# Optimization experiments

Hardware: AMD Instinct MI355X
Metric: run time of the kernel (lower is better)

## Reference

```python
import jax, jax.numpy as jnp
import numpy as np

P_FACTOR = 3.0
EPS = 1e-12  # torch F.normalize eps


def _l2_normalize(x):
    # matches torch.nn.functional.normalize(x, dim=-1): x / max(||x||, eps)
    n = jnp.linalg.norm(x, axis=-1, keepdims=True)
    return x / jnp.maximum(n, EPS)


def setup_inputs() -> dict:
    key = jax.random.key(0)
    k1, k2, k3 = jax.random.split(key, 3)
    N, D, H, C = 8192, 16384, 256, 28
    return {
        "features": jax.random.normal(k1, (N, H), dtype=jnp.float32),
        "ex_features": jax.random.normal(k2, (D, H), dtype=jnp.float32),
        "ex_class_reps": jax.random.normal(k3, (D, C), dtype=jnp.float32),
    }


def reference(features, ex_features, ex_class_reps):
    # cosine similarity: [N, D]
    s = _l2_normalize(features) @ _l2_normalize(ex_features).T
    # power-law activation: |s|^p * sign(s)
    a = jnp.power(jnp.abs(s), P_FACTOR) * jnp.sign(s)
    intensity = a.sum(axis=1)               # [N]
    echo = a @ ex_class_reps                # [N, C]
    return (echo, intensity)
```

## Files before the change

### kernel.cpp

```cpp
#include <hip/hip_runtime.h>
#include <stdint.h>


typedef unsigned short u16;
typedef __bf16 bf16x8 __attribute__((ext_vector_type(8)));
typedef float f32x4 __attribute__((ext_vector_type(4)));
typedef unsigned short u16x4 __attribute__((ext_vector_type(4)));

#define NQ 8192
#define ND 16384
#define NH 256
#define NC 28
#define DCHUNK 1024
#define NDT 8
#define NSLOT 16

__device__ __forceinline__ u16 f2bf(float f) {
  unsigned u = __builtin_bit_cast(unsigned, f);
  u += 0x7fffu + ((u >> 16) & 1u);
  return (u16)(u >> 16);
}

__device__ __forceinline__ unsigned cvtpk(float lo, float hi) {
  unsigned r;
  asm("v_cvt_pk_bf16_f32 %0, %1, %2" : "=v"(r) : "v"(lo), "v"(hi));
  return r;
}

__device__ __forceinline__ void swap2(unsigned& x, unsigned& y) {
  asm("v_permlane32_swap_b32 %0, %1" : "+v"(x), "+v"(y));
  asm("v_permlane16_swap_b32 %0, %1" : "+v"(x), "+v"(y));
}

__device__ __forceinline__ void gload16(const void* g, void* l) {
  __builtin_amdgcn_global_load_lds(
      (__attribute__((address_space(1))) void*)g,
      (__attribute__((address_space(3))) void*)l, 16, 0, 0);
}

__global__ __launch_bounds__(256) void norm_kernel(const float* __restrict__ in,
                                                   u16* __restrict__ out, int rows) {
  const int wid = threadIdx.x >> 6, lane = threadIdx.x & 63;
  const int row = blockIdx.x * 4 + wid;
  if (row >= rows) return;
  const float4* p = (const float4*)(in + (size_t)row * NH);
  float4 v = p[lane];
  float ss = v.x * v.x + v.y * v.y + v.z * v.z + v.w * v.w;
#pragma unroll
  for (int m = 1; m <= 32; m <<= 1) ss += __shfl_xor(ss, m, 64);
  const float sc = 1.0f / fmaxf(sqrtf(ss), 1e-12f);
  u16x4 o;
  o.x = f2bf(v.x * sc); o.y = f2bf(v.y * sc);
  o.z = f2bf(v.z * sc); o.w = f2bf(v.w * sc);
  *(u16x4*)(out + (size_t)row * NH + lane * 4) = o;
}

__global__ __launch_bounds__(256) void vt_kernel(const float* __restrict__ V,
                                                 u16* __restrict__ Vt) {
  const int d = blockIdx.x * 256 + threadIdx.x;
#pragma unroll
  for (int c = 0; c < NC; ++c) Vt[(size_t)c * ND + d] = f2bf(V[(size_t)d * NC + c]);
  Vt[(size_t)28 * ND + d] = 0x3F80;
  Vt[(size_t)29 * ND + d] = 0;
  Vt[(size_t)30 * ND + d] = 0;
  Vt[(size_t)31 * ND + d] = 0;
}

__global__ __launch_bounds__(256, 2) void fused_kernel(
    const u16* __restrict__ Qn, const u16* __restrict__ Kn,
    const u16* __restrict__ Vt, float* __restrict__ ep) {
  __shared__ alignas(16) char smem[32768];
  const int tid = threadIdx.x;
  const int wid = tid >> 6;
  const int lane = tid & 63;
  const int l16 = lane & 15;
  const int lg = lane >> 4;
  const int dch = blockIdx.x & 15;
  const int ntile = blockIdx.x >> 4;
  const int qbase = ntile * 128;
  const int rowbase = qbase + wid * 32;

  bf16x8 qA[2][8];
#pragma unroll
  for (int mb = 0; mb < 2; ++mb)
#pragma unroll
    for (int ks = 0; ks < 8; ++ks)
      qA[mb][ks] = *(const bf16x8*)(Qn + (size_t)(rowbase + mb * 16 + l16) * NH +
                                    ks * 32 + lg * 8);

  f32x4 eacc[2][2];
#pragma unroll
  for (int mb = 0; mb < 2; ++mb) {
    eacc[mb][0] = f32x4{0.f, 0.f, 0.f, 0.f};
    eacc[mb][1] = f32x4{0.f, 0.f, 0.f, 0.f};
  }
  f32x4 sacc[2][8];

  auto stageK = [&](int buf, int h0, const u16* kt) {
#pragma unroll
    for (int r = 0; r < 4; ++r) {
      const int row = r * 32 + (tid >> 3);
      const int c8 = (tid & 7) ^ (row & 7);
      gload16(kt + (size_t)row * NH + h0 + c8 * 8,
              smem + buf * 16384 + r * 4096 + wid * 1024);
    }
  };

  const u16* kc = Kn + (size_t)dch * DCHUNK * NH;
  stageK(0, 0, kc);
  __syncthreads();

  for (int t = 0; t < NDT; ++t) {
    const u16* kt = kc + (size_t)t * 128 * NH;
#pragma unroll
    for (int mb = 0; mb < 2; ++mb)
#pragma unroll
      for (int nb = 0; nb < 8; ++nb) sacc[mb][nb] = f32x4{0.f, 0.f, 0.f, 0.f};

#pragma unroll
    for (int ks = 0; ks < 4; ++ks) {
      if (ks < 3) stageK((ks + 1) & 1, (ks + 1) * 64, kt);
      else if (t < NDT - 1) stageK(0, 0, kt + 128 * NH);
      const char* kbuf = smem + (ks & 1) * 16384;
#pragma unroll
      for (int k2 = 0; k2 < 2; ++k2) {
        bf16x8 B[8];
#pragma unroll
        for (int nb = 0; nb < 8; ++nb)
          B[nb] = *(const bf16x8*)(kbuf + (nb * 16 + l16) * 128 +
                                   (((k2 * 4 + lg) ^ (l16 & 7)) << 4));
#pragma unroll
        for (int mb = 0; mb < 2; ++mb)
#pragma unroll
          for (int nb = 0; nb < 8; ++nb)
            sacc[mb][nb] = __builtin_amdgcn_mfma_f32_16x16x32_bf16(
                B[nb], qA[mb][ks * 2 + k2], sacc[mb][nb], 0, 0, 0);
      }
      __syncthreads();
    }

    const int dbase = dch * DCHUNK + t * 128;
#pragma unroll
    for (int mb = 0; mb < 2; ++mb) {
#pragma unroll
      for (int tg = 0; tg < 4; ++tg) {
        f32x4 sx = sacc[mb][2 * tg];
        f32x4 sy = sacc[mb][2 * tg + 1];
        f32x4 cx = sx * sx * sx;
        f32x4 cy = sy * sy * sy;
        unsigned x0 = cvtpk(cx[0], cx[1]);
        unsigned x1 = cvtpk(cx[2], cx[3]);
        unsigned y0 = cvtpk(cy[0], cy[1]);
        unsigned y1 = cvtpk(cy[2], cy[3]);
        swap2(x0, y0);
        swap2(x1, y1);
        const int4 ai = {(int)x0, (int)x1, (int)y0, (int)y1};
        const bf16x8 aA = __builtin_bit_cast(bf16x8, ai);
#pragma unroll
        for (int cn = 0; cn < 2; ++cn) {
          const bf16x8 vBf = *(const bf16x8*)(Vt + (size_t)(cn * 16 + l16) * ND +
                                              dbase + tg * 32 + lg * 8);
          eacc[mb][cn] = __builtin_amdgcn_mfma_f32_16x16x32_bf16(
              aA, vBf, eacc[mb][cn], 0, 0, 0);
        }
      }
    }
  }

#pragma unroll
  for (int mb = 0; mb < 2; ++mb)
#pragma unroll
    for (int cn = 0; cn < 2; ++cn)
#pragma unroll
      for (int r = 0; r < 4; ++r) {
        const int row = rowbase + mb * 16 + lg * 4 + r;
        ep[((size_t)dch * NQ + row) * 32 + cn * 16 + l16] = eacc[mb][cn][r];
      }
}

__global__ __launch_bounds__(256) void reduce_kernel(const float* __restrict__ ep,
                                                     float* __restrict__ out) {
  const int g = blockIdx.x * 256 + threadIdx.x;
  const int q = g >> 5, c = g & 31;
  if (c < NC) {
    float s = 0.f;
#pragma unroll
    for (int k = 0; k < NSLOT; ++k) s += ep[((size_t)k * NQ + q) * 32 + c];
    out[(size_t)q * NC + c] = s;
  } else if (c == NC) {
    float s = 0.f;
#pragma unroll
    for (int k = 0; k < NSLOT; ++k) s += ep[((size_t)k * NQ + q) * 32 + NC];
    out[(size_t)NQ * NC + q] = s;
  }
}

extern "C" void kernel_launch(void* const* d_in, const int* in_sizes, int n_in,
                              void* d_out, int out_size, void* d_ws, size_t ws_size,
                              hipStream_t stream) {
  const float* feat = (const float*)d_in[0];
  const float* exf  = (const float*)d_in[1];
  const float* exc  = (const float*)d_in[2];
  float* out = (float*)d_out;
  char* ws = (char*)d_ws;
  u16* qn = (u16*)ws;
  u16* kn = (u16*)(ws + 4194304);
  u16* vt = (u16*)(ws + 12582912);
  float* ep = (float*)(ws + 13631488);

  norm_kernel<<<dim3(NQ / 4), dim3(256), 0, stream>>>(feat, qn, NQ);
  norm_kernel<<<dim3(ND / 4), dim3(256), 0, stream>>>(exf, kn, ND);
  vt_kernel<<<dim3(ND / 256), dim3(256), 0, stream>>>(exc, vt);
  fused_kernel<<<dim3(1024), dim3(256), 0, stream>>>(qn, kn, vt, ep);
  reduce_kernel<<<dim3(NQ * 32 / 256), dim3(256), 0, stream>>>(ep, out);
}
```

Before: 98.21 us.

## Load K operands directly from global memory instead of staging through LDS

Removes the double-buffered global_load_lds staging of K tiles into shared memory and the per-step block barriers. Each wave now reads its B fragments for the MFMA directly from global memory (relying on L1/L2 for reuse across the four waves). This drops LDS usage and synchronization, but each wave issues redundant global loads for the same K tile and loses explicit prefetch overlap, so the loop may become latency-bound.

Result: slower. 289.6 us (+194.9%).

```diff
diff --git a/kernel.cpp b/kernel.cpp
--- a/kernel.cpp
+++ b/kernel.cpp
@@ -32,12 +32,6 @@
   asm("v_permlane16_swap_b32 %0, %1" : "+v"(x), "+v"(y));
 }
 
-__device__ __forceinline__ void gload16(const void* g, void* l) {
-  __builtin_amdgcn_global_load_lds(
-      (__attribute__((address_space(1))) void*)g,
-      (__attribute__((address_space(3))) void*)l, 16, 0, 0);
-}
-
 __global__ __launch_bounds__(256) void norm_kernel(const float* __restrict__ in,
                                                    u16* __restrict__ out, int rows) {
   const int wid = threadIdx.x >> 6, lane = threadIdx.x & 63;
@@ -69,7 +63,6 @@
 __global__ __launch_bounds__(256, 2) void fused_kernel(
     const u16* __restrict__ Qn, const u16* __restrict__ Kn,
     const u16* __restrict__ Vt, float* __restrict__ ep) {
-  __shared__ alignas(16) char smem[32768];
   const int tid = threadIdx.x;
   const int wid = tid >> 6;
   const int lane = tid & 63;
@@ -77,8 +70,7 @@
   const int lg = lane >> 4;
   const int dch = blockIdx.x & 15;
   const int ntile = blockIdx.x >> 4;
-  const int qbase = ntile * 128;
-  const int rowbase = qbase + wid * 32;
+  const int rowbase = ntile * 128 + wid * 32;
 
   bf16x8 qA[2][8];
 #pragma unroll
@@ -96,19 +88,7 @@
   }
   f32x4 sacc[2][8];
 
-  auto stageK = [&](int buf, int h0, const u16* kt) {
-#pragma unroll
-    for (int r = 0; r < 4; ++r) {
-      const int row = r * 32 + (tid >> 3);
-      const int c8 = (tid & 7) ^ (row & 7);
-      gload16(kt + (size_t)row * NH + h0 + c8 * 8,
-              smem + buf * 16384 + r * 4096 + wid * 1024);
-    }
-  };
-
   const u16* kc = Kn + (size_t)dch * DCHUNK * NH;
-  stageK(0, 0, kc);
-  __syncthreads();
 
   for (int t = 0; t < NDT; ++t) {
     const u16* kt = kc + (size_t)t * 128 * NH;
@@ -118,25 +98,21 @@
       for (int nb = 0; nb < 8; ++nb) sacc[mb][nb] = f32x4{0.f, 0.f, 0.f, 0.f};
 
 #pragma unroll
-    for (int ks = 0; ks < 4; ++ks) {
-      if (ks < 3) stageK((ks + 1) & 1, (ks + 1) * 64, kt);
-      else if (t < NDT - 1) stageK(0, 0, kt + 128 * NH);
-      const char* kbuf = smem + (ks & 1) * 16384;
+    for (int ks = 0; ks < 8; ++ks) {
 #pragma unroll
-      for (int k2 = 0; k2 < 2; ++k2) {
-        bf16x8 B[8];
+      for (int nh = 0; nh < 2; ++nh) {
+        bf16x8 B[4];
 #pragma unroll
-        for (int nb = 0; nb < 8; ++nb)
-          B[nb] = *(const bf16x8*)(kbuf + (nb * 16 + l16) * 128 +
-                                   (((k2 * 4 + lg) ^ (l16 & 7)) << 4));
+        for (int nb = 0; nb < 4; ++nb)
+          B[nb] = *(const bf16x8*)(kt + (size_t)((nh * 4 + nb) * 16 + l16) * NH +
+                                   ks * 32 + lg * 8);
 #pragma unroll
         for (int mb = 0; mb < 2; ++mb)
 #pragma unroll
-          for (int nb = 0; nb < 8; ++nb)
-            sacc[mb][nb] = __builtin_amdgcn_mfma_f32_16x16x32_bf16(
-                B[nb], qA[mb][ks * 2 + k2], sacc[mb][nb], 0, 0, 0);
+          for (int nb = 0; nb < 4; ++nb)
+            sacc[mb][nh * 4 + nb] = __builtin_amdgcn_mfma_f32_16x16x32_bf16(
+                B[nb], qA[mb][ks], sacc[mb][nh * 4 + nb], 0, 0, 0);
       }
-      __syncthreads();
     }
 
     const int dbase = dch * DCHUNK + t * 128;
```
